# Kernel tuning notes

Measured on AMD Instinct MI355X. Metric: run time of the kernel, lower is better.

## Reference

```python
import jax, jax.numpy as jnp
import numpy as np

# Model constants (match init_kwargs + mamba_ssm defaults)
CIN, COUT, K, STRIDE = 64, 128, 4, 4
D = 128            # d_model = features_out
DI = 256           # d_inner = 2*D (expand=2)
NSTATE = 16        # d_state
DCONV = 4          # depthwise conv width
DT_RANK = 8        # ceil(D/16)
NB = 3             # blocks per direction
NTOT = 2 * NB      # forward + backward stacks


def setup_inputs() -> dict:
    key = jax.random.key(0)
    ks = jax.random.split(key, 10)
    s = 0.02
    x = jax.random.normal(ks[0], (2, CIN, 8192), jnp.float32)
    convd_w = jax.random.normal(ks[1], (COUT, CIN, K), jnp.float32) * s
    convd_b = jnp.zeros((COUT,), jnp.float32)
    ln_w = jnp.ones((NTOT, D), jnp.float32)
    ln_b = jnp.zeros((NTOT, D), jnp.float32)
    in_proj_w = jax.random.normal(ks[2], (NTOT, 2 * DI, D), jnp.float32) * s
    conv_w = jax.random.normal(ks[3], (NTOT, DI, DCONV), jnp.float32) * s
    conv_b = jnp.zeros((NTOT, DI), jnp.float32)
    xproj_w = jax.random.normal(ks[4], (NTOT, DT_RANK + 2 * NSTATE, DI), jnp.float32) * s
    dtproj_w = jax.random.normal(ks[5], (NTOT, DI, DT_RANK), jnp.float32) * s
    dtproj_b = jax.random.normal(ks[6], (NTOT, DI), jnp.float32) * s
    # S4D-real init: A = -[1..N]
    A_log = jnp.log(jnp.broadcast_to(jnp.arange(1, NSTATE + 1, dtype=jnp.float32), (NTOT, DI, NSTATE)))
    Dparam = jnp.ones((NTOT, DI), jnp.float32)
    outproj_w = jax.random.normal(ks[7], (NTOT, D, DI), jnp.float32) * s
    return dict(x=x, convd_w=convd_w, convd_b=convd_b, ln_w=ln_w, ln_b=ln_b,
                in_proj_w=in_proj_w, conv_w=conv_w, conv_b=conv_b, xproj_w=xproj_w,
                dtproj_w=dtproj_w, dtproj_b=dtproj_b, A_log=A_log, Dparam=Dparam,
                outproj_w=outproj_w)


def _silu(x):
    return x * jax.nn.sigmoid(x)


def _layernorm(x, w, b, eps=1e-5):
    m = x.mean(-1, keepdims=True)
    xc = x - m
    v = (xc * xc).mean(-1, keepdims=True)
    return xc * jax.lax.rsqrt(v + eps) * w + b


def _mamba_mixer(x, in_proj_w, conv_w, conv_b, xproj_w, dtproj_w, dtproj_b, A_log, Dp, outproj_w):
    # x: (B, L, D)
    B, L, _ = x.shape
    xz = jnp.einsum('bld,ed->ble', x, in_proj_w)          # (B, L, 2*DI)
    xm, z = jnp.split(xz, 2, axis=-1)
    # causal depthwise conv (pad left DCONV-1, truncate to L)
    xp = jnp.pad(xm, ((0, 0), (DCONV - 1, 0), (0, 0)))
    xc = conv_b
    acc = jnp.zeros_like(xm)
    for k in range(DCONV):
        acc = acc + xp[:, k:k + L, :] * conv_w[:, k]
    xc = _silu(acc + conv_b)                               # (B, L, DI)
    dbc = jnp.einsum('ble,ne->bln', xc, xproj_w)           # (B, L, DT_RANK + 2N)
    dt, Bc, Cc = jnp.split(dbc, [DT_RANK, DT_RANK + NSTATE], axis=-1)
    dt = jax.nn.softplus(jnp.einsum('blr,dr->bld', dt, dtproj_w) + dtproj_b)  # (B, L, DI)
    A = -jnp.exp(A_log)                                    # (DI, N)
    dA = jnp.exp(dt[..., None] * A)                        # (B, L, DI, N)
    dBx = dt[..., None] * Bc[:, :, None, :] * xc[..., None]

    def step(h, inp):
        dA_t, dBx_t, C_t = inp
        h = dA_t * h + dBx_t                               # (B, DI, N)
        y = jnp.einsum('bdn,bn->bd', h, C_t)
        return h, y

    h0 = jnp.zeros((B, DI, NSTATE), x.dtype)
    _, ys = jax.lax.scan(step, h0, (jnp.swapaxes(dA, 0, 1), jnp.swapaxes(dBx, 0, 1), jnp.swapaxes(Cc, 0, 1)))
    y = jnp.swapaxes(ys, 0, 1)                             # (B, L, DI)
    y = (y + Dp * xc) * _silu(z)
    return jnp.einsum('ble,de->bld', y, outproj_w)         # (B, L, D)


def _mamba_stack(x, off, ln_w, ln_b, in_proj_w, conv_w, conv_b, xproj_w, dtproj_w, dtproj_b, A_log, Dparam, outproj_w):
    # mamba_ssm Block semantics: residual = x (+ prev residual); x = mixer(norm(residual))
    res = None
    cur = x
    for i in range(NB):
        j = off + i
        res = cur if res is None else cur + res
        hn = _layernorm(res, ln_w[j], ln_b[j])
        cur = _mamba_mixer(hn, in_proj_w[j], conv_w[j], conv_b[j], xproj_w[j],
                           dtproj_w[j], dtproj_b[j], A_log[j], Dparam[j], outproj_w[j])
    return cur, res


def reference(x, convd_w, convd_b, ln_w, ln_b, in_proj_w, conv_w, conv_b, xproj_w,
              dtproj_w, dtproj_b, A_log, Dparam, outproj_w):
    # downsampling conv + SiLU
    y = jax.lax.conv_general_dilated(x, convd_w, (STRIDE,), 'VALID',
                                     dimension_numbers=('NCH', 'OIH', 'NCH'))
    y = _silu(y + convd_b[None, :, None])                  # (B, COUT, L')
    h = jnp.swapaxes(y, 1, 2)                              # (B, L', D)
    xf, rf = _mamba_stack(h, 0, ln_w, ln_b, in_proj_w, conv_w, conv_b, xproj_w,
                          dtproj_w, dtproj_b, A_log, Dparam, outproj_w)
    xb, rb = _mamba_stack(h[:, ::-1, :], NB, ln_w, ln_b, in_proj_w, conv_w, conv_b, xproj_w,
                          dtproj_w, dtproj_b, A_log, Dparam, outproj_w)
    out = (xf + rf) + (xb + rb)[:, ::-1, :]
    return jnp.swapaxes(out, 1, 2), rf, rb
```

## Files before the change

### kernel.cpp

```cpp
#include <hip/hip_runtime.h>
#include <math.h>

#define B    2
#define CIN  64
#define LIN  8192
#define L    2048
#define D    128
#define DI   256
#define NS   16
#define RK   8
#define NSTREAM 4
#define CH   32
#define NCH  (L/CH)
#define TOK  (NSTREAM*L)
#define SZ_D ((size_t)TOK*D)
#define SZ_DI ((size_t)TOK*DI)
#define SXM 280
#define SHN 152

typedef short  bfrag __attribute__((ext_vector_type(8)));
typedef float  facc  __attribute__((ext_vector_type(4)));
#define MFMA __builtin_amdgcn_mfma_f32_16x16x32_bf16

__device__ __forceinline__ float sigmoidf_(float x){ return 1.f/(1.f+__expf(-x)); }
__device__ __forceinline__ float siluf_(float x){ return x*sigmoidf_(x); }
__device__ __forceinline__ ushort f2bf(float f){
    unsigned u = __float_as_uint(f);
    u += 0x7fffu + ((u>>16)&1u);
    return (ushort)(u>>16);
}
__device__ __forceinline__ float bf2f(ushort u){ return __uint_as_float(((unsigned)u)<<16); }
__device__ __forceinline__ float softplusf_(float t){
    return (t > 20.f) ? t : __logf(1.f + __expf(t));
}

__global__ void __launch_bounds__(256,1)
k_downcvt(const float* __restrict__ x, const float* __restrict__ convd_w,
          const float* __restrict__ bias,
          const float* __restrict__ ipw, const float* __restrict__ opw,
          const float* __restrict__ xpw,
          float* __restrict__ h, ushort* __restrict__ wall){
    int tid = threadIdx.x;
    if (blockIdx.x >= 128){
        int g = (blockIdx.x - 128)*256 + tid;
        for (int i = g; i < 688128; i += 32768){
            ushort v;
            if (i < 393216)      v = f2bf(ipw[i]);
            else if (i < 589824) v = f2bf(opw[i-393216]);
            else {
                int t = i - 589824;
                int k = t & 255, nr = (t>>8) & 63, jj = t>>14;
                v = (nr < 40) ? f2bf(xpw[((size_t)jj*40 + nr)*256 + k]) : (ushort)0;
            }
            wall[i] = v;
        }
        return;
    }
    __shared__ ushort sxd[64*SXM];
    __shared__ ushort swt[64*SXM];
    int mb = blockIdx.x & 63, nb = blockIdx.x >> 6;
    int m0 = mb*64;
    int b = m0 >> 11;
    int l0 = m0 & 2047;
    for (int idx = tid; idx < 64*64; idx += 256){
        int t = idx & 63, cc = idx >> 6;
        float4 v = *(const float4*)(x + ((size_t)(b*CIN + cc))*LIN + 4*(l0+t));
        ushort4 o; o.x=f2bf(v.x); o.y=f2bf(v.y); o.z=f2bf(v.z); o.w=f2bf(v.w);
        *(ushort4*)&sxd[t*SXM + cc*4] = o;
    }
    for (int idx = tid; idx < 64*64; idx += 256){
        int cl = idx >> 6, kq = idx & 63;
        float4 v = *(const float4*)(convd_w + ((size_t)(nb*64 + cl))*256 + kq*4);
        ushort4 o; o.x=f2bf(v.x); o.y=f2bf(v.y); o.z=f2bf(v.z); o.w=f2bf(v.w);
        *(ushort4*)&swt[cl*SXM + kq*4] = o;
    }
    __syncthreads();
    int w = tid>>6, lane = tid&63, rw = w>>1, cw_ = w&1;
    int q = lane>>4, r = lane&15;
    int n0 = nb*64 + cw_*32;
    facc acc[2][2] = {};
    #pragma unroll
    for (int kb=0; kb<8; ++kb){
        bfrag a0 = *(bfrag*)&sxd[(rw*32 + r)*SXM + kb*32 + q*8];
        bfrag a1 = *(bfrag*)&sxd[(rw*32 + 16 + r)*SXM + kb*32 + q*8];
        bfrag b0 = *(bfrag*)&swt[(cw_*32 + r)*SXM + kb*32 + q*8];
        bfrag b1 = *(bfrag*)&swt[(cw_*32 + 16 + r)*SXM + kb*32 + q*8];
        acc[0][0] = MFMA(a0,b0,acc[0][0],0,0,0);
        acc[0][1] = MFMA(a0,b1,acc[0][1],0,0,0);
        acc[1][0] = MFMA(a1,b0,acc[1][0],0,0,0);
        acc[1][1] = MFMA(a1,b1,acc[1][1],0,0,0);
    }
    #pragma unroll
    for (int im=0; im<2; ++im)
    #pragma unroll
    for (int in=0; in<2; ++in){
        int col = n0 + in*16 + r;
        float bv = bias[col];
        #pragma unroll
        for (int r2=0; r2<4; ++r2){
            int row = m0 + rw*32 + im*16 + q*4 + r2;
            int bb = row >> 11, l = row & 2047;
            float v = siluf_(acc[im][in][r2] + bv);
            h[((size_t)(bb*L + l))*D + col] = v;
            h[((size_t)((2+bb)*L + (L-1-l)))*D + col] = v;
        }
    }
}

__global__ void __launch_bounds__(512,1)
k_head(const float* __restrict__ curIn, const float* __restrict__ resIn,
       float* __restrict__ resOut,
       const float* __restrict__ lnw, const float* __restrict__ lnb,
       const ushort* __restrict__ wbi, const ushort* __restrict__ wbx,
       const float* __restrict__ cw, const float* __restrict__ cb,
       const float* __restrict__ Wdt, const float* __restrict__ bdt,
       const float* __restrict__ A_log,
       ushort* __restrict__ zh, ushort* __restrict__ xch,
       float* __restrict__ dtr, float* __restrict__ Bc, float* __restrict__ Cc,
       float* __restrict__ Aprod, float* __restrict__ Bend, int blk, int first){
    __shared__ ushort smHn[35*SHN];
    __shared__ ushort smXm[35*SXM];
    __shared__ ushort smXc[32*SXM];
    __shared__ float  smDbc[32*68];
    const int tid = threadIdx.x;
    const int bi = blockIdx.x;
    const int s = bi >> 6, c = bi & 63;
    const int j = (s>>1)*3 + blk;
    const int base_tok = s*L + c*CH;

    {
        int t = tid >> 4, g = tid & 15;
        size_t off = (size_t)(base_tok + t)*D + g*8;
        float4 v[2];
        const float4* cp = (const float4*)(curIn + off);
        v[0] = cp[0]; v[1] = cp[1];
        if (!first){
            const float4* rp = (const float4*)(resIn + off);
            #pragma unroll
            for (int i=0;i<2;++i){ float4 rv=rp[i]; v[i].x+=rv.x; v[i].y+=rv.y; v[i].z+=rv.z; v[i].w+=rv.w; }
        }
        {
            float4* ro = (float4*)(resOut + off);
            ro[0] = v[0]; ro[1] = v[1];
        }
        float s1=0.f, s2=0.f;
        #pragma unroll
        for (int i=0;i<2;++i){
            s1 += v[i].x+v[i].y+v[i].z+v[i].w;
            s2 += v[i].x*v[i].x+v[i].y*v[i].y+v[i].z*v[i].z+v[i].w*v[i].w;
        }
        s1 += __shfl_xor(s1,1); s2 += __shfl_xor(s2,1);
        s1 += __shfl_xor(s1,2); s2 += __shfl_xor(s2,2);
        s1 += __shfl_xor(s1,4); s2 += __shfl_xor(s2,4);
        s1 += __shfl_xor(s1,8); s2 += __shfl_xor(s2,8);
        float mean = s1*(1.f/128.f);
        float var  = s2*(1.f/128.f) - mean*mean;
        float rstd = rsqrtf(var + 1e-5f);
        const float4* lwp = (const float4*)(lnw + j*D + g*8);
        const float4* lbp = (const float4*)(lnb + j*D + g*8);
        #pragma unroll
        for (int i=0;i<2;++i){
            float4 lw = lwp[i], lb = lbp[i];
            ushort4 o;
            o.x = f2bf((v[i].x-mean)*rstd*lw.x + lb.x);
            o.y = f2bf((v[i].y-mean)*rstd*lw.y + lb.y);
            o.z = f2bf((v[i].z-mean)*rstd*lw.z + lb.z);
            o.w = f2bf((v[i].w-mean)*rstd*lw.w + lb.w);
            *(ushort4*)&smHn[t*SHN + g*8 + i*4] = o;
        }
    }
    if (c > 0 && tid < 48){
        int t = tid >> 4, g = tid & 15;
        size_t off = (size_t)(base_tok - 3 + t)*D + g*8;
        float4 v[2];
        const float4* cp = (const float4*)(curIn + off);
        v[0] = cp[0]; v[1] = cp[1];
        if (!first){
            const float4* rp = (const float4*)(resIn + off);
            #pragma unroll
            for (int i=0;i<2;++i){ float4 rv=rp[i]; v[i].x+=rv.x; v[i].y+=rv.y; v[i].z+=rv.z; v[i].w+=rv.w; }
        }
        float s1=0.f, s2=0.f;
        #pragma unroll
        for (int i=0;i<2;++i){
            s1 += v[i].x+v[i].y+v[i].z+v[i].w;
            s2 += v[i].x*v[i].x+v[i].y*v[i].y+v[i].z*v[i].z+v[i].w*v[i].w;
        }
        s1 += __shfl_xor(s1,1); s2 += __shfl_xor(s2,1);
        s1 += __shfl_xor(s1,2); s2 += __shfl_xor(s2,2);
        s1 += __shfl_xor(s1,4); s2 += __shfl_xor(s2,4);
        s1 += __shfl_xor(s1,8); s2 += __shfl_xor(s2,8);
        float mean = s1*(1.f/128.f);
        float var  = s2*(1.f/128.f) - mean*mean;
        float rstd = rsqrtf(var + 1e-5f);
        const float4* lwp = (const float4*)(lnw + j*D + g*8);
        const float4* lbp = (const float4*)(lnb + j*D + g*8);
        #pragma unroll
        for (int i=0;i<2;++i){
            float4 lw = lwp[i], lb = lbp[i];
            ushort4 o;
            o.x = f2bf((v[i].x-mean)*rstd*lw.x + lb.x);
            o.y = f2bf((v[i].y-mean)*rstd*lw.y + lb.y);
            o.z = f2bf((v[i].z-mean)*rstd*lw.z + lb.z);
            o.w = f2bf((v[i].w-mean)*rstd*lw.w + lb.w);
            *(ushort4*)&smHn[(32+t)*SHN + g*8 + i*4] = o;
        }
    }
    __syncthreads();

    {
        int w = tid>>6, lane = tid&63, q = lane>>4, r = lane&15;
        bfrag a[3][4];
        #pragma unroll
        for (int rt=0; rt<3; ++rt)
        #pragma unroll
        for (int kb=0; kb<4; ++kb)
            a[rt][kb] = *(bfrag*)&smHn[(rt*16 + r)*SHN + kb*32 + q*8];
        #pragma unroll
        for (int ct=0; ct<4; ++ct){
            int n0 = w*64 + ct*16;
            const ushort* bp = wbi + ((size_t)j*512 + n0 + r)*128 + q*8;
            facc a0 = {}, a1 = {}, a2 = {};
            #pragma unroll
            for (int kb=0; kb<4; ++kb){
                bfrag bv = *(const bfrag*)(bp + kb*32);
                a0 = MFMA(a[0][kb], bv, a0, 0,0,0);
                a1 = MFMA(a[1][kb], bv, a1, 0,0,0);
                a2 = MFMA(a[2][kb], bv, a2, 0,0,0);
            }
            int colL = n0 + r;
            if (colL < DI){
                #pragma unroll
                for (int r2=0;r2<4;++r2){
                    int rr = q*4 + r2;
                    smXm[rr*SXM + colL]      = f2bf(a0[r2]);
                    smXm[(16+rr)*SXM + colL] = f2bf(a1[r2]);
                    if (rr < 3) smXm[(32+rr)*SXM + colL] = f2bf(a2[r2]);
                }
            } else {
                int cz = colL - DI;
                #pragma unroll
                for (int r2=0;r2<4;++r2){
                    int rr = q*4 + r2;
                    zh[(size_t)(base_tok + rr)*DI + cz]      = f2bf(a0[r2]);
                    zh[(size_t)(base_tok + 16 + rr)*DI + cz] = f2bf(a1[r2]);
                }
            }
        }
    }
    __syncthreads();

    {
        int d = tid & 255, th = tid >> 8;
        const float* w4 = cw + ((size_t)j*DI + d)*4;
        float cw0=w4[0], cw1=w4[1], cw2=w4[2], cw3=w4[3];
        float cbb = cb[j*DI + d];
        float xm1, xm2, xm3;
        if (th == 0){
            xm1 = xm2 = xm3 = 0.f;
            if (c > 0){
                xm3 = bf2f(smXm[32*SXM + d]);
                xm2 = bf2f(smXm[33*SXM + d]);
                xm1 = bf2f(smXm[34*SXM + d]);
            }
        } else {
            xm3 = bf2f(smXm[13*SXM + d]);
            xm2 = bf2f(smXm[14*SXM + d]);
            xm1 = bf2f(smXm[15*SXM + d]);
        }
        int l0 = th*16;
        #pragma unroll 4
        for (int i=0;i<16;++i){
            int l = l0 + i;
            float x0 = bf2f(smXm[l*SXM + d]);
            float v = siluf_(cbb + cw3*x0 + cw2*xm1 + cw1*xm2 + cw0*xm3);
            ushort vb = f2bf(v);
            smXc[l*SXM + d] = vb;
            xch[(size_t)(base_tok+l)*DI + d] = vb;
            xm3 = xm2; xm2 = xm1; xm1 = x0;
        }
    }
    __syncthreads();

    if (tid < 256){
        int w = tid>>6, lane = tid&63, q = lane>>4, r = lane&15;
        facc a0 = {}, a1 = {};
        const ushort* bp = wbx + ((size_t)j*64 + w*16 + r)*256 + q*8;
        #pragma unroll
        for (int kb=0; kb<8; ++kb){
            bfrag av0 = *(bfrag*)&smXc[r*SXM + kb*32 + q*8];
            bfrag av1 = *(bfrag*)&smXc[(16+r)*SXM + kb*32 + q*8];
            bfrag bv  = *(const bfrag*)(bp + kb*32);
            a0 = MFMA(av0, bv, a0, 0,0,0);
            a1 = MFMA(av1, bv, a1, 0,0,0);
        }
        int col = w*16 + r;
        #pragma unroll
        for (int r2=0;r2<4;++r2){
            int rr = q*4 + r2;
            smDbc[rr*68 + col]      = a0[r2];
            smDbc[(16+rr)*68 + col] = a1[r2];
            int row0 = base_tok + rr, row1 = base_tok + 16 + rr;
            if      (col < 8){  dtr[(size_t)row0*RK + col] = a0[r2];      dtr[(size_t)row1*RK + col] = a1[r2]; }
            else if (col < 24){ Bc [(size_t)row0*NS + (col-8)] = a0[r2];  Bc [(size_t)row1*NS + (col-8)] = a1[r2]; }
            else if (col < 40){ Cc [(size_t)row0*NS + (col-24)] = a0[r2]; Cc [(size_t)row1*NS + (col-24)] = a1[r2]; }
        }
    }
    __syncthreads();

    {
        int d = tid & 255, hh = tid >> 8;
        float A[8], wv[RK];
        const float* ar = A_log + ((size_t)j*DI + d)*NS + hh*8;
        #pragma unroll
        for (int n=0;n<8;++n) A[n] = -__expf(ar[n]);
        const float* wr = Wdt + ((size_t)j*DI + d)*RK;
        #pragma unroll
        for (int r=0;r<RK;++r) wv[r] = wr[r];
        float bb2 = bdt[j*DI + d];
        float ap[8], hs[8];
        #pragma unroll
        for (int n=0;n<8;++n){ ap[n]=1.f; hs[n]=0.f; }
        #pragma unroll 4
        for (int l=0;l<CH;++l){
            float t = bb2;
            #pragma unroll
            for (int r=0;r<RK;++r) t += smDbc[l*68+r]*wv[r];
            float dtv = softplusf_(t);
            float xv  = bf2f(smXc[l*SXM + d]);
            float dbx = dtv*xv;
            #pragma unroll
            for (int n=0;n<8;++n){
                float dA = __expf(dtv*A[n]);
                ap[n] *= dA;
                hs[n] = dA*hs[n] + dbx*smDbc[l*68+8+hh*8+n];
            }
        }
        size_t pb = (size_t)bi*4096 + (size_t)d*16 + hh*8;
        #pragma unroll
        for (int k4=0;k4<2;++k4){
            float4 av, bv;
            av.x=ap[k4*4+0]; av.y=ap[k4*4+1]; av.z=ap[k4*4+2]; av.w=ap[k4*4+3];
            bv.x=hs[k4*4+0]; bv.y=hs[k4*4+1]; bv.z=hs[k4*4+2]; bv.w=hs[k4*4+3];
            *(float4*)&Aprod[pb + k4*4] = av;
            *(float4*)&Bend [pb + k4*4] = bv;
        }
    }
}

__global__ void k_scanmid(const float* __restrict__ Aprod, float* __restrict__ Bend){
    int tid = blockIdx.x*128 + threadIdx.x;
    int s = tid >> 12;
    int nd = tid & 4095;
    size_t base = (size_t)s*NCH*4096 + nd;
    float h = 0.f;
    for (int c0=0; c0<NCH; c0+=16){
        float a[16], b[16];
        #pragma unroll
        for (int i=0;i<16;++i){
            a[i] = Aprod[base + (size_t)(c0+i)*4096];
            b[i] = Bend [base + (size_t)(c0+i)*4096];
        }
        #pragma unroll
        for (int i=0;i<16;++i){
            Bend[base + (size_t)(c0+i)*4096] = h;
            h = a[i]*h + b[i];
        }
    }
}

__global__ void __launch_bounds__(512,1)
k_tail(const float* __restrict__ dtr, const ushort* __restrict__ xch,
       const float* __restrict__ Bc, const float* __restrict__ Cc,
       const float* __restrict__ A_log,
       const float* __restrict__ Wdt, const float* __restrict__ bdt,
       const float* __restrict__ h0, const ushort* __restrict__ zh,
       const float* __restrict__ Dp, const ushort* __restrict__ wbo,
       float* __restrict__ cur, int blk){
    int c = blockIdx.x, s = blockIdx.y; int j = (s>>1)*3 + blk;
    int tid = threadIdx.x;
    __shared__ float sB[CH*NS], sC[CH*NS], sdtr[CH*RK];
    __shared__ ushort sg[CH*SXM];
    int base_tok = s*L + c*CH;
    sB[tid] = Bc[(size_t)base_tok*NS + tid];
    sC[tid] = Cc[(size_t)base_tok*NS + tid];
    if (tid < 256) sdtr[tid] = dtr[(size_t)base_tok*RK + tid];
    int d = tid >> 1, hh = tid & 1;
    float A[8], wv[RK];
    const float* ar = A_log + ((size_t)j*DI + d)*NS + hh*8;
    #pragma unroll
    for (int n=0;n<8;++n) A[n] = -__expf(ar[n]);
    const float* wr = Wdt + ((size_t)j*DI + d)*RK;
    #pragma unroll
    for (int r=0;r<RK;++r) wv[r] = wr[r];
    float bb = bdt[j*DI + d];
    float Dpd = Dp[j*DI + d];
    float hs[8];
    {
        size_t pb = (size_t)(s*NCH + c)*4096 + (size_t)d*16 + hh*8;
        float4 h0v0 = *(const float4*)&h0[pb];
        float4 h0v1 = *(const float4*)&h0[pb+4];
        hs[0]=h0v0.x; hs[1]=h0v0.y; hs[2]=h0v0.z; hs[3]=h0v0.w;
        hs[4]=h0v1.x; hs[5]=h0v1.y; hs[6]=h0v1.z; hs[7]=h0v1.w;
    }
    __syncthreads();
    #pragma unroll 4
    for (int l=0;l<CH;++l){
        float t = bb;
        #pragma unroll
        for (int r=0;r<RK;++r) t += sdtr[l*RK+r]*wv[r];
        float dtv = softplusf_(t);
        float xv  = bf2f(xch[(size_t)(base_tok+l)*DI + d]);
        float dbx = dtv*xv;
        float p = 0.f;
        #pragma unroll
        for (int n=0;n<8;++n){
            float dA = __expf(dtv*A[n]);
            hs[n] = dA*hs[n] + dbx*sB[l*NS+hh*8+n];
            p += hs[n]*sC[l*NS+hh*8+n];
        }
        p += __shfl_xor(p, 1);
        if (hh == 0){
            float zv = bf2f(zh[(size_t)(base_tok+l)*DI + d]);
            sg[l*SXM + d] = f2bf((p + Dpd*xv)*siluf_(zv));
        }
    }
    __syncthreads();
    int w = tid>>6, lane = tid&63, q = lane>>4, r = lane&15;
    facc acc0 = {}, acc1 = {};
    const ushort* b0p = wbo + ((size_t)j*128 + w*16 + r)*256 + q*8;
    #pragma unroll
    for (int kb=0; kb<8; ++kb){
        bfrag av0 = *(bfrag*)&sg[r*SXM + kb*32 + q*8];
        bfrag av1 = *(bfrag*)&sg[(16+r)*SXM + kb*32 + q*8];
        bfrag bv0 = *(const bfrag*)(b0p + kb*32);
        acc0 = MFMA(av0,bv0,acc0,0,0,0);
        acc1 = MFMA(av1,bv0,acc1,0,0,0);
    }
    int col = w*16 + r;
    #pragma unroll
    for (int r2=0;r2<4;++r2){
        int row0 = base_tok + q*4 + r2;
        cur[(size_t)row0*D + col]      = acc0[r2];
        cur[(size_t)(row0+16)*D + col] = acc1[r2];
    }
}

__global__ void k_final(const float* __restrict__ cur, const float* __restrict__ res,
                        float* __restrict__ out){
    int l = blockIdx.x, b = blockIdx.y, d = threadIdx.x;
    int tf = (b*L + l)*D + d;
    int tbk = ((2+b)*L + (L-1-l))*D + d;
    float f  = cur[tf] + res[tf];
    float bw = cur[tbk] + res[tbk];
    out[((size_t)(b*D + d))*L + l] = f + bw;
    out[(size_t)2*D*L + (size_t)(b*L + l)*D + d] = res[tf];
    out[(size_t)2*D*L + (size_t)((2+b)*L + l)*D + d] = res[((2+b)*L + l)*D + d];
}

extern "C" void kernel_launch(void* const* d_in, const int* in_sizes, int n_in,
                              void* d_out, int out_size, void* d_ws, size_t ws_size,
                              hipStream_t stream){
    const float* x         = (const float*)d_in[0];
    const float* convd_w   = (const float*)d_in[1];
    const float* convd_b   = (const float*)d_in[2];
    const float* ln_w      = (const float*)d_in[3];
    const float* ln_b      = (const float*)d_in[4];
    const float* in_proj_w = (const float*)d_in[5];
    const float* conv_w    = (const float*)d_in[6];
    const float* conv_b    = (const float*)d_in[7];
    const float* xproj_w   = (const float*)d_in[8];
    const float* dtproj_w  = (const float*)d_in[9];
    const float* dtproj_b  = (const float*)d_in[10];
    const float* A_log     = (const float*)d_in[11];
    const float* Dparam    = (const float*)d_in[12];
    const float* outproj_w = (const float*)d_in[13];

    float* ws = (float*)d_ws;
    float* h     = ws; ws += SZ_D;
    float* res0  = ws; ws += SZ_D;
    float* res1  = ws; ws += SZ_D;
    float* cur   = ws; ws += SZ_D;
    ushort* zh   = (ushort*)ws; ws += SZ_DI/2;
    ushort* xch  = (ushort*)ws; ws += SZ_DI/2;
    float* Aprod = ws; ws += SZ_D;
    float* Bend  = ws; ws += SZ_D;
    float* dtr   = ws; ws += (size_t)TOK*RK;
    float* Bc    = ws; ws += (size_t)TOK*NS;
    float* Cc    = ws; ws += (size_t)TOK*NS;
    ushort* wall = (ushort*)ws;
    ushort* wbi  = wall;
    ushort* wbo  = wall + 393216;
    ushort* wbx  = wall + 589824;

    k_downcvt<<<256, 256, 0, stream>>>(x, convd_w, convd_b, in_proj_w, outproj_w,
                                       xproj_w, h, wall);

    float* resin[3]  = { nullptr, res0, res1 };
    float* resout[3] = { res0,    res1, res0 };
    for (int blk = 0; blk < 3; ++blk){
        const float* ci = (blk==0) ? h : cur;
        const float* ri = (blk==0) ? h : resin[blk];
        k_head<<<NSTREAM*NCH, 512, 0, stream>>>(ci, ri, resout[blk], ln_w, ln_b, wbi, wbx,
                                                conv_w, conv_b, dtproj_w, dtproj_b, A_log,
                                                zh, xch, dtr, Bc, Cc, Aprod, Bend, blk, blk==0);
        k_scanmid<<<128, 128, 0, stream>>>(Aprod, Bend);
        k_tail<<<dim3(NCH, NSTREAM), 512, 0, stream>>>(dtr, xch, Bc, Cc, A_log,
                                                       dtproj_w, dtproj_b, Bend, zh,
                                                       Dparam, wbo, cur, blk);
    }

    k_final<<<dim3(L, B), 128, 0, stream>>>(cur, res0, (float*)d_out);
}
```

Before: 264.8 us.

## Fuse chunk-scan carry into head via last-block atomic; fold residual into tail

Removes the separate k_scanmid launch. The last-arriving block per stream, found through an atomic counter, now runs the sequential inter-chunk prefix over Aprod/Bend. The residual add is moved from the head of the next block into the tail's output-projection epilogue, which writes r = out + r_in directly. This eliminates the cur/res double reads and writes. k_final is rewritten to transpose through shared memory for coalesced output stores. The cost is a serial fold done by a single block per stream, plus a memset for the counters.

```diff
diff --git a/kernel.cpp b/kernel.cpp
--- a/kernel.cpp
+++ b/kernel.cpp
@@ -108,8 +108,7 @@
 }
 
 __global__ void __launch_bounds__(512,1)
-k_head(const float* __restrict__ curIn, const float* __restrict__ resIn,
-       float* __restrict__ resOut,
+k_head(const float* __restrict__ rIn,
        const float* __restrict__ lnw, const float* __restrict__ lnb,
        const ushort* __restrict__ wbi, const ushort* __restrict__ wbx,
        const float* __restrict__ cw, const float* __restrict__ cb,
@@ -117,11 +116,13 @@
        const float* __restrict__ A_log,
        ushort* __restrict__ zh, ushort* __restrict__ xch,
        float* __restrict__ dtr, float* __restrict__ Bc, float* __restrict__ Cc,
-       float* __restrict__ Aprod, float* __restrict__ Bend, int blk, int first){
+       float* __restrict__ Ap, float* __restrict__ Bp,
+       unsigned* __restrict__ cnt, int blk){
     __shared__ ushort smHn[35*SHN];
     __shared__ ushort smXm[35*SXM];
     __shared__ ushort smXc[32*SXM];
     __shared__ float  smDbc[32*68];
+    __shared__ int    sFold;
     const int tid = threadIdx.x;
     const int bi = blockIdx.x;
     const int s = bi >> 6, c = bi & 63;
@@ -131,18 +132,8 @@
     {
         int t = tid >> 4, g = tid & 15;
         size_t off = (size_t)(base_tok + t)*D + g*8;
-        float4 v[2];
-        const float4* cp = (const float4*)(curIn + off);
-        v[0] = cp[0]; v[1] = cp[1];
-        if (!first){
-            const float4* rp = (const float4*)(resIn + off);
-            #pragma unroll
-            for (int i=0;i<2;++i){ float4 rv=rp[i]; v[i].x+=rv.x; v[i].y+=rv.y; v[i].z+=rv.z; v[i].w+=rv.w; }
-        }
-        {
-            float4* ro = (float4*)(resOut + off);
-            ro[0] = v[0]; ro[1] = v[1];
-        }
+        const float4* cp = (const float4*)(rIn + off);
+        float4 v[2]; v[0] = cp[0]; v[1] = cp[1];
         float s1=0.f, s2=0.f;
         #pragma unroll
         for (int i=0;i<2;++i){
@@ -172,14 +163,8 @@
     if (c > 0 && tid < 48){
         int t = tid >> 4, g = tid & 15;
         size_t off = (size_t)(base_tok - 3 + t)*D + g*8;
-        float4 v[2];
-        const float4* cp = (const float4*)(curIn + off);
-        v[0] = cp[0]; v[1] = cp[1];
-        if (!first){
-            const float4* rp = (const float4*)(resIn + off);
-            #pragma unroll
-            for (int i=0;i<2;++i){ float4 rv=rp[i]; v[i].x+=rv.x; v[i].y+=rv.y; v[i].z+=rv.z; v[i].w+=rv.w; }
-        }
+        const float4* cp = (const float4*)(rIn + off);
+        float4 v[2]; v[0] = cp[0]; v[1] = cp[1];
         float s1=0.f, s2=0.f;
         #pragma unroll
         for (int i=0;i<2;++i){
@@ -337,34 +322,46 @@
             }
         }
         size_t pb = (size_t)bi*4096 + (size_t)d*16 + hh*8;
-        #pragma unroll
-        for (int k4=0;k4<2;++k4){
-            float4 av, bv;
-            av.x=ap[k4*4+0]; av.y=ap[k4*4+1]; av.z=ap[k4*4+2]; av.w=ap[k4*4+3];
-            bv.x=hs[k4*4+0]; bv.y=hs[k4*4+1]; bv.z=hs[k4*4+2]; bv.w=hs[k4*4+3];
-            *(float4*)&Aprod[pb + k4*4] = av;
-            *(float4*)&Bend [pb + k4*4] = bv;
-        }
-    }
-}
-
-__global__ void k_scanmid(const float* __restrict__ Aprod, float* __restrict__ Bend){
-    int tid = blockIdx.x*128 + threadIdx.x;
-    int s = tid >> 12;
-    int nd = tid & 4095;
-    size_t base = (size_t)s*NCH*4096 + nd;
-    float h = 0.f;
-    for (int c0=0; c0<NCH; c0+=16){
-        float a[16], b[16];
-        #pragma unroll
-        for (int i=0;i<16;++i){
-            a[i] = Aprod[base + (size_t)(c0+i)*4096];
-            b[i] = Bend [base + (size_t)(c0+i)*4096];
-        }
-        #pragma unroll
-        for (int i=0;i<16;++i){
-            Bend[base + (size_t)(c0+i)*4096] = h;
-            h = a[i]*h + b[i];
+        float4 av0, bv0;
+        av0.x=ap[0];av0.y=ap[1];av0.z=ap[2];av0.w=ap[3];
+        bv0.x=hs[0];bv0.y=hs[1];bv0.z=hs[2];bv0.w=hs[3];
+        *(float4*)&Ap[pb]   = av0;
+        *(float4*)&Bp[pb]   = bv0;
+        av0.x=ap[4];av0.y=ap[5];av0.z=ap[6];av0.w=ap[7];
+        bv0.x=hs[4];bv0.y=hs[5];bv0.z=hs[6];bv0.w=hs[7];
+        *(float4*)&Ap[pb+4] = av0;
+        *(float4*)&Bp[pb+4] = bv0;
+    }
+    __syncthreads();
+
+    if (tid == 0){
+        __threadfence();
+        unsigned old = atomicAdd(&cnt[s], 1u);
+        sFold = (old == (unsigned)(NCH-1));
+    }
+    __syncthreads();
+    if (sFold){
+        if (tid == 0) __threadfence();
+        __syncthreads();
+        size_t sb = (size_t)(s*NCH)*4096 + (size_t)tid*8;
+        float4 hA = {0.f,0.f,0.f,0.f}, hB = {0.f,0.f,0.f,0.f};
+        for (int c4 = 0; c4 < NCH; c4 += 4){
+            float4 a[4][2], b4[4][2];
+            #pragma unroll
+            for (int u=0;u<4;++u){
+                const float4* apv = (const float4*)&Ap[sb + (size_t)(c4+u)*4096];
+                const float4* bpv = (const float4*)&Bp[sb + (size_t)(c4+u)*4096];
+                a[u][0]=apv[0]; a[u][1]=apv[1]; b4[u][0]=bpv[0]; b4[u][1]=bpv[1];
+            }
+            #pragma unroll
+            for (int u=0;u<4;++u){
+                float4* wp = (float4*)&Bp[sb + (size_t)(c4+u)*4096];
+                wp[0] = hA; wp[1] = hB;
+                hA.x = a[u][0].x*hA.x + b4[u][0].x; hA.y = a[u][0].y*hA.y + b4[u][0].y;
+                hA.z = a[u][0].z*hA.z + b4[u][0].z; hA.w = a[u][0].w*hA.w + b4[u][0].w;
+                hB.x = a[u][1].x*hB.x + b4[u][1].x; hB.y = a[u][1].y*hB.y + b4[u][1].y;
+                hB.z = a[u][1].z*hB.z + b4[u][1].z; hB.w = a[u][1].w*hB.w + b4[u][1].w;
+            }
         }
     }
 }
@@ -376,7 +373,7 @@
        const float* __restrict__ Wdt, const float* __restrict__ bdt,
        const float* __restrict__ h0, const ushort* __restrict__ zh,
        const float* __restrict__ Dp, const ushort* __restrict__ wbo,
-       float* __restrict__ cur, int blk){
+       const float* __restrict__ rIn, float* __restrict__ rOut, int blk){
     int c = blockIdx.x, s = blockIdx.y; int j = (s>>1)*3 + blk;
     int tid = threadIdx.x;
     __shared__ float sB[CH*NS], sC[CH*NS], sdtr[CH*RK];
@@ -441,21 +438,37 @@
     #pragma unroll
     for (int r2=0;r2<4;++r2){
         int row0 = base_tok + q*4 + r2;
-        cur[(size_t)row0*D + col]      = acc0[r2];
-        cur[(size_t)(row0+16)*D + col] = acc1[r2];
-    }
-}
-
-__global__ void k_final(const float* __restrict__ cur, const float* __restrict__ res,
-                        float* __restrict__ out){
-    int l = blockIdx.x, b = blockIdx.y, d = threadIdx.x;
-    int tf = (b*L + l)*D + d;
-    int tbk = ((2+b)*L + (L-1-l))*D + d;
-    float f  = cur[tf] + res[tf];
-    float bw = cur[tbk] + res[tbk];
-    out[((size_t)(b*D + d))*L + l] = f + bw;
-    out[(size_t)2*D*L + (size_t)(b*L + l)*D + d] = res[tf];
-    out[(size_t)2*D*L + (size_t)((2+b)*L + l)*D + d] = res[((2+b)*L + l)*D + d];
+        size_t i0 = (size_t)row0*D + col;
+        size_t i1 = (size_t)(row0+16)*D + col;
+        rOut[i0] = acc0[r2] + rIn[i0];
+        rOut[i1] = acc1[r2] + rIn[i1];
+    }
+}
+
+__global__ void __launch_bounds__(256,1)
+k_final(const float* __restrict__ r3, const float* __restrict__ r2,
+        float* __restrict__ out){
+    __shared__ float sf[128*33];
+    int b = blockIdx.y, l0 = blockIdx.x*32;
+    int tid = threadIdx.x;
+    #pragma unroll
+    for (int k=0;k<16;++k){
+        int idx = tid + k*256;
+        int l = l0 + (idx>>7), d = idx&127;
+        int tf  = (b*L + l)*D + d;
+        int tbk = ((2+b)*L + (L-1-l))*D + d;
+        float f = r3[tf] + r3[tbk];
+        sf[d*33 + (l-l0)] = f;
+        out[(size_t)2*D*L + tf] = r2[tf];
+        out[(size_t)2*D*L + (size_t)((2+b)*L + l)*D + d] = r2[((2+b)*L + l)*D + d];
+    }
+    __syncthreads();
+    #pragma unroll
+    for (int k=0;k<16;++k){
+        int idx = tid + k*256;
+        int d = idx>>5, li = idx&31;
+        out[((size_t)(b*D + d))*L + l0 + li] = sf[d*33 + li];
+    }
 }
 
 extern "C" void kernel_launch(void* const* d_in, const int* in_sizes, int n_in,
@@ -478,37 +491,37 @@
 
     float* ws = (float*)d_ws;
     float* h     = ws; ws += SZ_D;
-    float* res0  = ws; ws += SZ_D;
-    float* res1  = ws; ws += SZ_D;
-    float* cur   = ws; ws += SZ_D;
+    float* r1    = ws; ws += SZ_D;
+    float* r2    = ws; ws += SZ_D;
+    float* r3    = ws; ws += SZ_D;
     ushort* zh   = (ushort*)ws; ws += SZ_DI/2;
     ushort* xch  = (ushort*)ws; ws += SZ_DI/2;
-    float* Aprod = ws; ws += SZ_D;
-    float* Bend  = ws; ws += SZ_D;
+    float* Ap    = ws; ws += SZ_D;
+    float* Bp    = ws; ws += SZ_D;
     float* dtr   = ws; ws += (size_t)TOK*RK;
-    float* Bc    = ws; ws += (size_t)TOK*NS;
-    float* Cc    = ws; ws += (size_t)TOK*NS;
+    float* Bcv   = ws; ws += (size_t)TOK*NS;
+    float* Ccv   = ws; ws += (size_t)TOK*NS;
+    unsigned* cnts = (unsigned*)ws; ws += 16;
     ushort* wall = (ushort*)ws;
     ushort* wbi  = wall;
     ushort* wbo  = wall + 393216;
     ushort* wbx  = wall + 589824;
 
+    hipMemsetAsync((void*)cnts, 0, 48, stream);
     k_downcvt<<<256, 256, 0, stream>>>(x, convd_w, convd_b, in_proj_w, outproj_w,
                                        xproj_w, h, wall);
 
-    float* resin[3]  = { nullptr, res0, res1 };
-    float* resout[3] = { res0,    res1, res0 };
+    const float* rin[3]  = { h,  r1, r2 };
+    float*       rout[3] = { r1, r2, r3 };
     for (int blk = 0; blk < 3; ++blk){
-        const float* ci = (blk==0) ? h : cur;
-        const float* ri = (blk==0) ? h : resin[blk];
-        k_head<<<NSTREAM*NCH, 512, 0, stream>>>(ci, ri, resout[blk], ln_w, ln_b, wbi, wbx,
+        k_head<<<NSTREAM*NCH, 512, 0, stream>>>(rin[blk], ln_w, ln_b, wbi, wbx,
                                                 conv_w, conv_b, dtproj_w, dtproj_b, A_log,
-                                                zh, xch, dtr, Bc, Cc, Aprod, Bend, blk, blk==0);
-        k_scanmid<<<128, 128, 0, stream>>>(Aprod, Bend);
-        k_tail<<<dim3(NCH, NSTREAM), 512, 0, stream>>>(dtr, xch, Bc, Cc, A_log,
-                                                       dtproj_w, dtproj_b, Bend, zh,
-                                                       Dparam, wbo, cur, blk);
-    }
-
-    k_final<<<dim3(L, B), 128, 0, stream>>>(cur, res0, (float*)d_out);
-}
+                                                zh, xch, dtr, Bcv, Ccv, Ap, Bp,
+                                                cnts + blk*4, blk);
+        k_tail<<<dim3(NCH, NSTREAM), 512, 0, stream>>>(dtr, xch, Bcv, Ccv, A_log,
+                                                       dtproj_w, dtproj_b, Bp, zh,
+                                                       Dparam, wbo, rin[blk], rout[blk], blk);
+    }
+
+    k_final<<<dim3(NCH, B), 256, 0, stream>>>(r3, r2, (float*)d_out);
+}
```

After: 400.1 us. +51.1%, slower.
